# Optimization experiments

Hardware: AMD Instinct MI355X
Metric: run time of the kernel (lower is better)

Reference implementation:

```python
import jax, jax.numpy as jnp
import numpy as np

TAIL_BOUND = 3.0
MIN_BIN_W = 1e-3
MIN_BIN_H = 1e-3
MIN_DERIV = 1e-3


def _rq_spline_fwd(x, uw, uh, us):
    # unconstrained rational-quadratic spline (Durkan et al., 'linear' tails)
    # x: [N, C]; uw, uh: [C, B]; us: [C, B-1]
    C, B = uw.shape
    dt = x.dtype
    inside = (x >= -TAIL_BOUND) & (x <= TAIL_BOUND)
    xc = jnp.clip(x, -TAIL_BOUND, TAIL_BOUND)

    widths = MIN_BIN_W + (1.0 - MIN_BIN_W * B) * jax.nn.softmax(uw, axis=-1)
    cumw = jnp.concatenate([jnp.zeros((C, 1), dt), jnp.cumsum(widths, -1)], -1)
    cumw = 2.0 * TAIL_BOUND * cumw - TAIL_BOUND
    cumw = cumw.at[:, 0].set(-TAIL_BOUND).at[:, -1].set(TAIL_BOUND)
    widths = cumw[:, 1:] - cumw[:, :-1]

    heights = MIN_BIN_H + (1.0 - MIN_BIN_H * B) * jax.nn.softmax(uh, axis=-1)
    cumh = jnp.concatenate([jnp.zeros((C, 1), dt), jnp.cumsum(heights, -1)], -1)
    cumh = 2.0 * TAIL_BOUND * cumh - TAIL_BOUND
    cumh = cumh.at[:, 0].set(-TAIL_BOUND).at[:, -1].set(TAIL_BOUND)
    heights = cumh[:, 1:] - cumh[:, :-1]

    # boundary derivative logits -> softplus(const) = 1 - MIN_DERIV
    const = float(np.log(np.expm1(1.0 - MIN_DERIV)))
    ud = jnp.concatenate([jnp.full((C, 1), const, dt), us,
                          jnp.full((C, 1), const, dt)], -1)
    derivs = MIN_DERIV + jax.nn.softplus(ud)  # [C, B+1]

    # searchsorted on bin x-edges (eps shift on last edge, as in reference impl)
    edges = cumw.at[:, -1].add(1e-6)
    idx = jnp.clip(jnp.sum(xc[:, :, None] >= edges[None, :, :], -1) - 1, 0, B - 1)  # [N, C]

    ci = jnp.arange(C)[None, :]
    xk = cumw[ci, idx]
    wk = widths[ci, idx]
    yk = cumh[ci, idx]
    hk = heights[ci, idx]
    dk = derivs[ci, idx]
    dk1 = derivs[ci, idx + 1]
    delta = hk / wk

    theta = (xc - xk) / wk
    t1m = theta * (1.0 - theta)
    num = hk * (delta * theta * theta + dk * t1m)
    den = delta + (dk + dk1 - 2.0 * delta) * t1m
    y = yk + num / den
    dnum = delta * delta * (dk1 * theta * theta + 2.0 * delta * t1m
                            + dk * (1.0 - theta) * (1.0 - theta))
    logdet = jnp.log(dnum) - 2.0 * jnp.log(den)

    # identity (log-det 0) outside the interval
    return jnp.where(inside, y, x), jnp.where(inside, logdet, jnp.zeros_like(logdet))


def setup_inputs() -> dict:
    key = jax.random.key(0)
    ks = jax.random.split(key, 6)
    N, L, C, B = 1000000, 8, 8, 32
    return {
        "x": jax.random.normal(ks[0], (N,), jnp.float32),
        "w": jax.random.normal(ks[1], (L, C, B), jnp.float32),
        "h": jax.random.normal(ks[2], (L, C, B), jnp.float32),
        "s": jax.random.normal(ks[3], (L, C, B - 1), jnp.float32),
        "bias": jax.random.normal(ks[4], (L + 1, C), jnp.float32),
        "log_scale": jax.random.normal(ks[5], (L + 1, C), jnp.float32),
    }


def reference(x, w, h, s, bias, log_scale):
    L, C = w.shape[0], w.shape[1]
    z = jnp.broadcast_to(x[:, None], (x.shape[0], C))
    log_j = jnp.zeros_like(z)
    for step in range(L):
        z = (z - bias[step]) * jnp.exp(-log_scale[step])
        z, ld = _rq_spline_fwd(z, w[step], h[step], s[step])
        log_j = log_j + ld - log_scale[step]
    z = (z - bias[L]) * jnp.exp(-log_scale[L])
    return z, log_j - log_scale[L]
```

## Files before the change

### kernel.cpp

```cpp
#include <hip/hip_runtime.h>
#include <hip/hip_bf16.h>


#define TB 3.0f
#define NB 32
#define NC 8
#define NL 8
#define LN2 0.69314718055994530942f

#define GX0 -6.5f
#define GX1 6.5f
#define TZ 0.5f
#define TL 0.5f

#define PT_FLOATS (64 * 99)
#define GP_FLOATS (PT_FLOATS + 72 + 72 + 8)
#define GP_BYTES  (GP_FLOATS * 4)
#define TAB_OFF   26112

__device__ __forceinline__ float softplusf(float v) {
    return fmaxf(v, 0.f) + log1pf(expf(-fabsf(v)));
}

__device__ __forceinline__ unsigned short f2h(float f) {
    _Float16 h = (_Float16)f;
    unsigned short u;
    __builtin_memcpy(&u, &h, 2);
    return u;
}
__device__ __forceinline__ float h2f(unsigned short u) {
    _Float16 h;
    __builtin_memcpy(&h, &u, 2);
    return (float)h;
}

__device__ __forceinline__ int bsearch32(const float* __restrict__ E, float xc) {
    int i = (xc >= E[16]) ? 16 : 0;
    i += (xc >= E[i + 8]) ? 8 : 0;
    i += (xc >= E[i + 4]) ? 4 : 0;
    i += (xc >= E[i + 2]) ? 2 : 0;
    i += (xc >= E[i + 1]) ? 1 : 0;
    return i;
}

__device__ __forceinline__ void spline_eval(const float* __restrict__ Tlc,
                                            float zc, float& zo, float& ldo) {
    const float* E  = Tlc;
    const float* Hc = Tlc + 33;
    const float* Dv = Tlc + 66;

    float xc = fminf(fmaxf(zc, -TB), TB);
    int i = bsearch32(E, xc);

    float xk  = E[i],  xk1 = E[i + 1];
    float yk  = Hc[i], yk1 = Hc[i + 1];
    float dk  = Dv[i], dk1 = Dv[i + 1];

    float wk    = xk1 - xk;
    float hk    = yk1 - yk;
    float invw  = __builtin_amdgcn_rcpf(wk);
    float delta = hk * invw;
    float th    = (xc - xk) * invw;
    float omt   = 1.f - th;
    float t1m   = th * omt;
    float th2   = th * th;

    float num    = hk * fmaf(delta, th2, dk * t1m);
    float den    = fmaf(fmaf(-2.f, delta, dk + dk1), t1m, delta);
    float invden = __builtin_amdgcn_rcpf(den);
    float y      = fmaf(num, invden, yk);

    float dt    = delta * t1m;
    float inner = fmaf(dk1, th2, fmaf(dk, omt * omt, dt + dt));
    float dnum  = (delta * delta) * inner;
    float r  = dnum * invden * invden;
    float ld = LN2 * __builtin_amdgcn_logf(r);

    bool inside = (zc >= -TB) && (zc <= TB);
    zo  = inside ? y : zc;
    ldo = inside ? ld : 0.f;
}

extern "C" __global__ void __launch_bounds__(256)
build_tables(const float* __restrict__ w, const float* __restrict__ h,
             const float* __restrict__ s, const float* __restrict__ bias,
             const float* __restrict__ lsc, float* __restrict__ gparam)
{
    __shared__ float T[PT_FLOATS];
    __shared__ float Sc[72], Bb[72], LJ[8];

    const int tid = threadIdx.x;

    if (tid < 64) {
        const int l = tid >> 3, c = tid & 7;
        float* cw = &T[tid * 99];
        const float* wr = w + (l * NC + c) * NB;
        float m = wr[0];
        for (int b = 1; b < NB; ++b) m = fmaxf(m, wr[b]);
        float sum = 0.f;
        for (int b = 0; b < NB; ++b) sum += expf(wr[b] - m);
        float inv = 1.f / sum;
        float acc = 0.f;
        cw[0] = -TB;
        for (int b = 0; b < NB; ++b) {
            acc += 1e-3f + (1.f - 1e-3f * NB) * (expf(wr[b] - m) * inv);
            cw[b + 1] = 6.f * acc - 3.f;
        }
        cw[NB] = TB;
    } else if (tid < 128) {
        const int t = tid - 64;
        float* ch = &T[t * 99 + 33];
        const int l = t >> 3, c = t & 7;
        const float* hr = h + (l * NC + c) * NB;
        float m = hr[0];
        for (int b = 1; b < NB; ++b) m = fmaxf(m, hr[b]);
        float sum = 0.f;
        for (int b = 0; b < NB; ++b) sum += expf(hr[b] - m);
        float inv = 1.f / sum;
        float acc = 0.f;
        ch[0] = -TB;
        for (int b = 0; b < NB; ++b) {
            acc += 1e-3f + (1.f - 1e-3f * NB) * (expf(hr[b] - m) * inv);
            ch[b + 1] = 6.f * acc - 3.f;
        }
        ch[NB] = TB;
    } else if (tid < 192) {
        const int t = tid - 128;
        const int l = t >> 3, c = t & 7;
        float* dv = &T[t * 99 + 66];
        const float* sr = s + (l * NC + c) * (NB - 1);
        const float cst = logf(expm1f(1.f - 1e-3f));
        const float dbound = 1e-3f + softplusf(cst);
        dv[0]  = dbound;
        dv[NB] = dbound;
        for (int k = 0; k < NB - 1; ++k)
            dv[k + 1] = 1e-3f + softplusf(sr[k]);
    }
    if (tid < 72) { Sc[tid] = expf(-lsc[tid]); Bb[tid] = bias[tid]; }
    if (tid < 8) {
        float a = 0.f;
        for (int l = 0; l <= NL; ++l) a += lsc[l * NC + tid];
        LJ[tid] = -a;
    }
    __syncthreads();

    for (int k = tid; k < PT_FLOATS; k += 256) gparam[k] = T[k];
    if (tid < 72) gparam[PT_FLOATS + tid]       = Sc[tid];
    if (tid < 72) gparam[PT_FLOATS + 72 + tid]  = Bb[tid];
    if (tid < 8)  gparam[PT_FLOATS + 144 + tid] = LJ[tid];
}

extern "C" __global__ void __launch_bounds__(256)
grid_eval(const float* __restrict__ gparam, char* __restrict__ tabb,
          int G, float dx)
{
    __shared__ float T[GP_FLOATS];
    __shared__ unsigned short ZL[256 * 16];
    for (int k = threadIdx.x; k < GP_FLOATS; k += 256) T[k] = gparam[k];
    __syncthreads();
    const float* ScT = T + PT_FLOATS;
    const float* BbT = ScT + 72;
    const float* LJT = BbT + 72;

    const int t  = threadIdx.x;
    const int p0 = blockIdx.x * 255;
    const int i  = min(p0 + t, G - 1);

    const float xv = fmaf((float)i, dx, GX0);
    float z[NC], lj[NC];
#pragma unroll
    for (int c = 0; c < NC; ++c) { z[c] = xv; lj[c] = LJT[c]; }

#pragma unroll 1
    for (int l = 0; l < NL; ++l) {
        const float* Tl = T + l * NC * 99;
#pragma unroll
        for (int c = 0; c < NC; ++c) {
            float u = (z[c] - BbT[l * 8 + c]) * ScT[l * 8 + c];
            float zo, ld;
            spline_eval(Tl + c * 99, u, zo, ld);
            z[c] = zo;
            lj[c] += ld;
        }
    }
    unsigned short zh[NC], lh[NC];
#pragma unroll
    for (int c = 0; c < NC; ++c) {
        z[c] = (z[c] - BbT[NL * 8 + c]) * ScT[NL * 8 + c];
        zh[c] = f2h(z[c]);
        lh[c] = f2h(lj[c]);
        ZL[t * 16 + c]     = zh[c];
        ZL[t * 16 + 8 + c] = lh[c];
    }
    __syncthreads();

    const int r = p0 + t;
    if (t < 255 && r <= G - 2) {
        ushort4* rowp = (ushort4*)(tabb + (size_t)r * 64);
#pragma unroll
        for (int c = 0; c < NC; ++c) {
            const float zn  = h2f(ZL[(t + 1) * 16 + c]);
            const float ljn = h2f(ZL[(t + 1) * 16 + 8 + c]);
            ushort4 v;
            v.x = zh[c]; v.y = f2h(zn - h2f(zh[c]));
            v.z = lh[c]; v.w = f2h(ljn - h2f(lh[c]));
            rowp[c] = v;
        }
    }
}

extern "C" __global__ void __launch_bounds__(256)
interp_kernel(const float* __restrict__ x, const char* __restrict__ tabb,
              float* __restrict__ out,
              unsigned* __restrict__ wcnt, unsigned* __restrict__ wl,
              int N, int G, float dx, float invdx)
{
    const int n   = blockIdx.x * 256 + threadIdx.x;
    const int wid = n >> 6;
    if (n >= N) return;

    const float xv = x[n];
    int i = (int)floorf((xv - GX0) * invdx);
    const bool oor = !(xv > GX0 && xv < GX1);
    i = min(max(i, 0), G - 2);
    const float t = (xv - fmaf((float)i, dx, GX0)) * invdx;

    const float4* rp = (const float4*)(tabb + (size_t)i * 64);
    union { float4 q[4]; unsigned int u[16]; } R;
    R.q[0] = rp[0]; R.q[1] = rp[1]; R.q[2] = rp[2]; R.q[3] = rp[3];

    float z[NC], lj[NC];
    int flags = 0;
#pragma unroll
    for (int c = 0; c < NC; ++c) {
        const unsigned a = R.u[2 * c], b = R.u[2 * c + 1];
        const float z0 = h2f((unsigned short)a);
        const float dz = h2f((unsigned short)(a >> 16));
        const float l0 = h2f((unsigned short)b);
        const float dl = h2f((unsigned short)(b >> 16));
        z[c]  = fmaf(t, dz, z0);
        lj[c] = fmaf(t, dl, l0);
        if (fabsf(dz) > TZ || fabsf(dl) > TL) flags |= (1 << c);
    }
    if (oor) flags = 0xff;

    const unsigned long long act = __ballot(1);
    const unsigned long long m   = __ballot(flags != 0);
    const int lane = threadIdx.x & 63;
    if (flags) {
        const int rank = __popcll(m & ((1ull << lane) - 1ull));
        wl[(size_t)wid * 64 + rank] = ((unsigned)n << 8) | (unsigned)flags;
    }
    if (lane == __ffsll((long long)act) - 1)
        wcnt[wid] = (unsigned)__popcll(m);

    float4* oz = (float4*)(out + (size_t)n * NC);
    oz[0] = make_float4(z[0], z[1], z[2], z[3]);
    oz[1] = make_float4(z[4], z[5], z[6], z[7]);
    float4* ol = (float4*)(out + (size_t)N * NC + (size_t)n * NC);
    ol[0] = make_float4(lj[0], lj[1], lj[2], lj[3]);
    ol[1] = make_float4(lj[4], lj[5], lj[6], lj[7]);
}

extern "C" __global__ void __launch_bounds__(256)
exact_kernel(const float* __restrict__ x, const float* __restrict__ gparam,
             const unsigned* __restrict__ wcnt, const unsigned* __restrict__ wl,
             int nwl, float* __restrict__ out, int N)
{
    __shared__ float T[GP_FLOATS];
    for (int k = threadIdx.x; k < GP_FLOATS; k += 256) T[k] = gparam[k];
    __syncthreads();
    const float* ScT = T + PT_FLOATS;
    const float* BbT = ScT + 72;
    const float* LJT = BbT + 72;

    const int lane = threadIdx.x & 63;
    const int wloc = threadIdx.x >> 6;
    for (int W = blockIdx.x * 4 + wloc; W < nwl; W += (int)gridDim.x * 4) {
        const unsigned cnt = min(wcnt[W], 64u);
        for (unsigned p = 0; p < cnt; p += 8) {
            const unsigned eidx = p + (unsigned)(lane >> 3);
            if (eidx >= cnt) continue;
            const unsigned ent = wl[(size_t)W * 64 + eidx];
            const int c = lane & 7;
            if (!((ent >> c) & 1u)) continue;
            const int n = (int)(ent >> 8);
            if (n >= N) continue;
            const float xv = x[n];
            float zc = xv;
            float lacc = LJT[c];
#pragma unroll 1
            for (int l = 0; l < NL; ++l) {
                zc = (zc - BbT[l * 8 + c]) * ScT[l * 8 + c];
                float ld;
                spline_eval(T + (l * 8 + c) * 99, zc, zc, ld);
                lacc += ld;
            }
            zc = (zc - BbT[NL * 8 + c]) * ScT[NL * 8 + c];
            out[(size_t)n * NC + c] = zc;
            out[(size_t)N * NC + (size_t)n * NC + c] = lacc;
        }
    }
}

extern "C" __global__ void __launch_bounds__(256)
flow_kernel(const float* __restrict__ x, const float* __restrict__ w,
            const float* __restrict__ h, const float* __restrict__ s,
            const float* __restrict__ bias, const float* __restrict__ lsc,
            float* __restrict__ out, int N)
{
    __shared__ float T[PT_FLOATS];
    __shared__ float Bb[NL + 1][NC];
    __shared__ float Sc[NL + 1][NC];
    __shared__ float LJC[NC];

    const int tid = threadIdx.x;
    if (tid < 64) {
        const int l = tid >> 3, c = tid & 7;
        float* cw = &T[tid * 99];
        {
            const float* wr = w + (l * NC + c) * NB;
            float m = wr[0];
            for (int b = 1; b < NB; ++b) m = fmaxf(m, wr[b]);
            float sum = 0.f;
            for (int b = 0; b < NB; ++b) sum += expf(wr[b] - m);
            float inv = 1.f / sum;
            float acc = 0.f;
            cw[0] = -TB;
            for (int b = 0; b < NB; ++b) {
                acc += 1e-3f + (1.f - 1e-3f * NB) * (expf(wr[b] - m) * inv);
                cw[b + 1] = 6.f * acc - 3.f;
            }
            cw[NB] = TB;
        }
        {
            float* ch = cw + 33;
            const float* hr = h + (l * NC + c) * NB;
            float m = hr[0];
            for (int b = 1; b < NB; ++b) m = fmaxf(m, hr[b]);
            float sum = 0.f;
            for (int b = 0; b < NB; ++b) sum += expf(hr[b] - m);
            float inv = 1.f / sum;
            float acc = 0.f;
            ch[0] = -TB;
            for (int b = 0; b < NB; ++b) {
                acc += 1e-3f + (1.f - 1e-3f * NB) * (expf(hr[b] - m) * inv);
                ch[b + 1] = 6.f * acc - 3.f;
            }
            ch[NB] = TB;
        }
        {
            float* dv = cw + 66;
            const float* sr = s + (l * NC + c) * (NB - 1);
            const float cst = logf(expm1f(1.f - 1e-3f));
            const float dbound = 1e-3f + softplusf(cst);
            dv[0]  = dbound;
            dv[NB] = dbound;
            for (int k = 0; k < NB - 1; ++k)
                dv[k + 1] = 1e-3f + softplusf(sr[k]);
        }
    }
    if (tid < (NL + 1) * NC) {
        const int l = tid >> 3, c = tid & 7;
        Bb[l][c] = bias[tid];
        Sc[l][c] = expf(-lsc[tid]);
    }
    if (tid < NC) {
        float a = 0.f;
        for (int l = 0; l <= NL; ++l) a += lsc[l * NC + tid];
        LJC[tid] = -a;
    }
    __syncthreads();

    const int n = blockIdx.x * 256 + tid;
    if (n >= N) return;
    const float xv = x[n];
    float z[NC], lj[NC];
#pragma unroll
    for (int c = 0; c < NC; ++c) { z[c] = xv; lj[c] = LJC[c]; }
#pragma unroll 1
    for (int l = 0; l < NL; ++l) {
        const float* Tl = &T[l * NC * 99];
#pragma unroll
        for (int c = 0; c < NC; ++c) {
            float zc = (z[c] - Bb[l][c]) * Sc[l][c];
            float zo, ld;
            spline_eval(Tl + c * 99, zc, zo, ld);
            z[c] = zo;
            lj[c] += ld;
        }
    }
#pragma unroll
    for (int c = 0; c < NC; ++c) z[c] = (z[c] - Bb[NL][c]) * Sc[NL][c];

    float4* oz = (float4*)(out + (size_t)n * NC);
    oz[0] = make_float4(z[0], z[1], z[2], z[3]);
    oz[1] = make_float4(z[4], z[5], z[6], z[7]);
    float4* ol = (float4*)(out + (size_t)N * NC + (size_t)n * NC);
    ol[0] = make_float4(lj[0], lj[1], lj[2], lj[3]);
    ol[1] = make_float4(lj[4], lj[5], lj[6], lj[7]);
}

extern "C" void kernel_launch(void* const* d_in, const int* in_sizes, int n_in,
                              void* d_out, int out_size, void* d_ws, size_t ws_size,
                              hipStream_t stream) {
    const float* x    = (const float*)d_in[0];
    const float* w    = (const float*)d_in[1];
    const float* h    = (const float*)d_in[2];
    const float* s    = (const float*)d_in[3];
    const float* bias = (const float*)d_in[4];
    const float* lsc  = (const float*)d_in[5];
    float* out = (float*)d_out;
    const int N = in_sizes[0];

    const int nwl = (N + 63) / 64;
    int G = 65536;
    while (G > 2048 &&
           ((size_t)TAB_OFF + (size_t)G * 64 + (size_t)nwl * 260) > ws_size)
        G >>= 1;
    const size_t tabEnd = (size_t)TAB_OFF + (size_t)G * 64;
    const size_t need   = tabEnd + (size_t)nwl * 260;

    if (need <= ws_size) {
        char* basep = (char*)d_ws;
        float*    gparam = (float*)basep;
        char*     tabb   = basep + TAB_OFF;
        unsigned* wcnt   = (unsigned*)(basep + tabEnd);
        unsigned* wl     = (unsigned*)(basep + tabEnd + (size_t)nwl * 4);

        const float dx = (GX1 - GX0) / (float)(G - 1);
        const int gblocks = (G - 1 + 254) / 255;
        build_tables<<<1, 256, 0, stream>>>(w, h, s, bias, lsc, gparam);
        grid_eval<<<gblocks, 256, 0, stream>>>(gparam, tabb, G, dx);
        interp_kernel<<<(N + 255) / 256, 256, 0, stream>>>(
            x, tabb, out, wcnt, wl, N, G, dx, 1.f / dx);
        exact_kernel<<<(nwl + 3) / 4, 256, 0, stream>>>(
            x, gparam, wcnt, wl, nwl, out, N);
    } else {
        flow_kernel<<<(N + 255) / 256, 256, 0, stream>>>(
            x, w, h, s, bias, lsc, out, N);
    }
}
```

Before: 70.90 us.

## Fuse exact fallback into interp kernel with block-local per-channel compaction

Measured after the change: 63.91 us. 9.9% less time.

```diff
diff --git a/kernel.cpp b/kernel.cpp
--- a/kernel.cpp
+++ b/kernel.cpp
@@ -17,6 +17,7 @@
 #define GP_FLOATS (PT_FLOATS + 72 + 72 + 8)
 #define GP_BYTES  (GP_FLOATS * 4)
 #define TAB_OFF   26112
+#define CAP 256
 
 __device__ __forceinline__ float softplusf(float v) {
     return fmaxf(v, 0.f) + log1pf(expf(-fabsf(v)));
@@ -79,6 +80,25 @@
     bool inside = (zc >= -TB) && (zc <= TB);
     zo  = inside ? y : zc;
     ldo = inside ? ld : 0.f;
+}
+
+__device__ __forceinline__ void exact_chain(const float* __restrict__ T,
+                                            float xv, int c,
+                                            float& zout, float& lout) {
+    const float* ScT = T + PT_FLOATS;
+    const float* BbT = ScT + 72;
+    const float* LJT = BbT + 72;
+    float zc = xv;
+    float lacc = LJT[c];
+#pragma unroll 1
+    for (int l = 0; l < NL; ++l) {
+        zc = (zc - BbT[l * 8 + c]) * ScT[l * 8 + c];
+        float ld;
+        spline_eval(T + (l * 8 + c) * 99, zc, zc, ld);
+        lacc += ld;
+    }
+    zout = (zc - BbT[NL * 8 + c]) * ScT[NL * 8 + c];
+    lout = lacc;
 }
 
 extern "C" __global__ void __launch_bounds__(256)
@@ -211,95 +231,117 @@
 
 extern "C" __global__ void __launch_bounds__(256)
 interp_kernel(const float* __restrict__ x, const char* __restrict__ tabb,
-              float* __restrict__ out,
-              unsigned* __restrict__ wcnt, unsigned* __restrict__ wl,
+              const float* __restrict__ gparam, float* __restrict__ out,
               int N, int G, float dx, float invdx)
 {
-    const int n   = blockIdx.x * 256 + threadIdx.x;
-    const int wid = n >> 6;
-    if (n >= N) return;
-
-    const float xv = x[n];
-    int i = (int)floorf((xv - GX0) * invdx);
-    const bool oor = !(xv > GX0 && xv < GX1);
-    i = min(max(i, 0), G - 2);
-    const float t = (xv - fmaf((float)i, dx, GX0)) * invdx;
-
-    const float4* rp = (const float4*)(tabb + (size_t)i * 64);
-    union { float4 q[4]; unsigned int u[16]; } R;
-    R.q[0] = rp[0]; R.q[1] = rp[1]; R.q[2] = rp[2]; R.q[3] = rp[3];
+    __shared__ float T[GP_FLOATS];
+    __shared__ float xbuf[256];
+    __shared__ unsigned short pairs[CAP];
+    __shared__ float resZ[CAP], resL[CAP];
+    __shared__ unsigned wsum[4];
+
+    const int tid  = threadIdx.x;
+    const int n    = blockIdx.x * 256 + tid;
+    const int lane = tid & 63;
+    const int wloc = tid >> 6;
+    const bool active = (n < N);
+
+    float xv = 0.f;
+    if (active) xv = x[n];
+    xbuf[tid] = xv;
 
     float z[NC], lj[NC];
     int flags = 0;
+    if (active) {
+        int i = (int)floorf((xv - GX0) * invdx);
+        const bool oor = !(xv > GX0 && xv < GX1);
+        i = min(max(i, 0), G - 2);
+        const float t = (xv - fmaf((float)i, dx, GX0)) * invdx;
+
+        const float4* rp = (const float4*)(tabb + (size_t)i * 64);
+        union { float4 q[4]; unsigned int u[16]; } R;
+        R.q[0] = rp[0]; R.q[1] = rp[1]; R.q[2] = rp[2]; R.q[3] = rp[3];
+#pragma unroll
+        for (int c = 0; c < NC; ++c) {
+            const unsigned a = R.u[2 * c], b = R.u[2 * c + 1];
+            const float z0 = h2f((unsigned short)a);
+            const float dz = h2f((unsigned short)(a >> 16));
+            const float l0 = h2f((unsigned short)b);
+            const float dl = h2f((unsigned short)(b >> 16));
+            z[c]  = fmaf(t, dz, z0);
+            lj[c] = fmaf(t, dl, l0);
+            if (fabsf(dz) > TZ || fabsf(dl) > TL) flags |= (1 << c);
+        }
+        if (oor) flags = 0xff;
+    }
+
+    unsigned long long m[NC];
+    unsigned wtot = 0;
 #pragma unroll
     for (int c = 0; c < NC; ++c) {
-        const unsigned a = R.u[2 * c], b = R.u[2 * c + 1];
-        const float z0 = h2f((unsigned short)a);
-        const float dz = h2f((unsigned short)(a >> 16));
-        const float l0 = h2f((unsigned short)b);
-        const float dl = h2f((unsigned short)(b >> 16));
-        z[c]  = fmaf(t, dz, z0);
-        lj[c] = fmaf(t, dl, l0);
-        if (fabsf(dz) > TZ || fabsf(dl) > TL) flags |= (1 << c);
-    }
-    if (oor) flags = 0xff;
-
-    const unsigned long long act = __ballot(1);
-    const unsigned long long m   = __ballot(flags != 0);
-    const int lane = threadIdx.x & 63;
-    if (flags) {
-        const int rank = __popcll(m & ((1ull << lane) - 1ull));
-        wl[(size_t)wid * 64 + rank] = ((unsigned)n << 8) | (unsigned)flags;
-    }
-    if (lane == __ffsll((long long)act) - 1)
-        wcnt[wid] = (unsigned)__popcll(m);
-
-    float4* oz = (float4*)(out + (size_t)n * NC);
-    oz[0] = make_float4(z[0], z[1], z[2], z[3]);
-    oz[1] = make_float4(z[4], z[5], z[6], z[7]);
-    float4* ol = (float4*)(out + (size_t)N * NC + (size_t)n * NC);
-    ol[0] = make_float4(lj[0], lj[1], lj[2], lj[3]);
-    ol[1] = make_float4(lj[4], lj[5], lj[6], lj[7]);
-}
-
-extern "C" __global__ void __launch_bounds__(256)
-exact_kernel(const float* __restrict__ x, const float* __restrict__ gparam,
-             const unsigned* __restrict__ wcnt, const unsigned* __restrict__ wl,
-             int nwl, float* __restrict__ out, int N)
-{
-    __shared__ float T[GP_FLOATS];
-    for (int k = threadIdx.x; k < GP_FLOATS; k += 256) T[k] = gparam[k];
-    __syncthreads();
-    const float* ScT = T + PT_FLOATS;
-    const float* BbT = ScT + 72;
-    const float* LJT = BbT + 72;
-
-    const int lane = threadIdx.x & 63;
-    const int wloc = threadIdx.x >> 6;
-    for (int W = blockIdx.x * 4 + wloc; W < nwl; W += (int)gridDim.x * 4) {
-        const unsigned cnt = min(wcnt[W], 64u);
-        for (unsigned p = 0; p < cnt; p += 8) {
-            const unsigned eidx = p + (unsigned)(lane >> 3);
-            if (eidx >= cnt) continue;
-            const unsigned ent = wl[(size_t)W * 64 + eidx];
-            const int c = lane & 7;
-            if (!((ent >> c) & 1u)) continue;
-            const int n = (int)(ent >> 8);
-            if (n >= N) continue;
-            const float xv = x[n];
-            float zc = xv;
-            float lacc = LJT[c];
-#pragma unroll 1
-            for (int l = 0; l < NL; ++l) {
-                zc = (zc - BbT[l * 8 + c]) * ScT[l * 8 + c];
-                float ld;
-                spline_eval(T + (l * 8 + c) * 99, zc, zc, ld);
-                lacc += ld;
+        m[c] = __ballot((flags >> c) & 1);
+        wtot += (unsigned)__popcll(m[c]);
+    }
+    if (lane == 0) wsum[wloc] = wtot;
+    __syncthreads();
+
+    unsigned woff = 0, btot = 0;
+#pragma unroll
+    for (int j = 0; j < 4; ++j) {
+        const unsigned v = wsum[j];
+        if (j < wloc) woff += v;
+        btot += v;
+    }
+    const unsigned long long lowmask = (1ull << lane) - 1ull;
+    {
+        unsigned basec = 0;
+#pragma unroll
+        for (int c = 0; c < NC; ++c) {
+            if ((flags >> c) & 1) {
+                const unsigned idx = woff + basec + (unsigned)__popcll(m[c] & lowmask);
+                if (idx < CAP) pairs[idx] = (unsigned short)((tid << 3) | c);
             }
-            zc = (zc - BbT[NL * 8 + c]) * ScT[NL * 8 + c];
-            out[(size_t)n * NC + c] = zc;
-            out[(size_t)N * NC + (size_t)n * NC + c] = lacc;
-        }
+            basec += (unsigned)__popcll(m[c]);
+        }
+    }
+    if (btot > 0) {
+        for (int k = tid; k < GP_FLOATS; k += 256) T[k] = gparam[k];
+    }
+    __syncthreads();
+
+    const unsigned pcnt = min(btot, (unsigned)CAP);
+    for (unsigned k = tid; k < pcnt; k += 256) {
+        const unsigned pr = pairs[k];
+        const int stid = (int)(pr >> 3), c = (int)(pr & 7u);
+        float zo, lo;
+        exact_chain(T, xbuf[stid], c, zo, lo);
+        resZ[k] = zo; resL[k] = lo;
+    }
+    __syncthreads();
+
+    if (active && flags) {
+        unsigned basec = 0;
+#pragma unroll
+        for (int c = 0; c < NC; ++c) {
+            if ((flags >> c) & 1) {
+                const unsigned idx = woff + basec + (unsigned)__popcll(m[c] & lowmask);
+                if (idx < CAP) {
+                    z[c] = resZ[idx]; lj[c] = resL[idx];
+                } else {
+                    exact_chain(T, xv, c, z[c], lj[c]);
+                }
+            }
+            basec += (unsigned)__popcll(m[c]);
+        }
+    }
+
+    if (active) {
+        float4* oz = (float4*)(out + (size_t)n * NC);
+        oz[0] = make_float4(z[0], z[1], z[2], z[3]);
+        oz[1] = make_float4(z[4], z[5], z[6], z[7]);
+        float4* ol = (float4*)(out + (size_t)N * NC + (size_t)n * NC);
+        ol[0] = make_float4(lj[0], lj[1], lj[2], lj[3]);
+        ol[1] = make_float4(lj[4], lj[5], lj[6], lj[7]);
     }
 }
 
@@ -413,29 +455,22 @@
     float* out = (float*)d_out;
     const int N = in_sizes[0];
 
-    const int nwl = (N + 63) / 64;
     int G = 65536;
-    while (G > 2048 &&
-           ((size_t)TAB_OFF + (size_t)G * 64 + (size_t)nwl * 260) > ws_size)
+    while (G > 2048 && ((size_t)TAB_OFF + (size_t)G * 64) > ws_size)
         G >>= 1;
-    const size_t tabEnd = (size_t)TAB_OFF + (size_t)G * 64;
-    const size_t need   = tabEnd + (size_t)nwl * 260;
+    const size_t need = (size_t)TAB_OFF + (size_t)G * 64;
 
     if (need <= ws_size) {
         char* basep = (char*)d_ws;
-        float*    gparam = (float*)basep;
-        char*     tabb   = basep + TAB_OFF;
-        unsigned* wcnt   = (unsigned*)(basep + tabEnd);
-        unsigned* wl     = (unsigned*)(basep + tabEnd + (size_t)nwl * 4);
+        float* gparam = (float*)basep;
+        char*  tabb   = basep + TAB_OFF;
 
         const float dx = (GX1 - GX0) / (float)(G - 1);
         const int gblocks = (G - 1 + 254) / 255;
         build_tables<<<1, 256, 0, stream>>>(w, h, s, bias, lsc, gparam);
         grid_eval<<<gblocks, 256, 0, stream>>>(gparam, tabb, G, dx);
         interp_kernel<<<(N + 255) / 256, 256, 0, stream>>>(
-            x, tabb, out, wcnt, wl, N, G, dx, 1.f / dx);
-        exact_kernel<<<(nwl + 3) / 4, 256, 0, stream>>>(
-            x, gparam, wcnt, wl, nwl, out, N);
+            x, tabb, gparam, out, N, G, dx, 1.f / dx);
     } else {
         flow_kernel<<<(N + 255) / 256, 256, 0, stream>>>(
             x, w, h, s, bias, lsc, out, N);
```

## Split interpolation and exact fallback work per point-channel pair

Applied to the files above, without the earlier changes.

Measured after the change: 98.83 us. 39.4% more time.

```diff
diff --git a/kernel.cpp b/kernel.cpp
--- a/kernel.cpp
+++ b/kernel.cpp
@@ -79,6 +79,25 @@
     bool inside = (zc >= -TB) && (zc <= TB);
     zo  = inside ? y : zc;
     ldo = inside ? ld : 0.f;
+}
+
+__device__ __forceinline__ void exact_chain(const float* __restrict__ T,
+                                            float xv, int c,
+                                            float& zout, float& lout) {
+    const float* ScT = T + PT_FLOATS;
+    const float* BbT = ScT + 72;
+    const float* LJT = BbT + 72;
+    float zc = xv;
+    float lacc = LJT[c];
+#pragma unroll 1
+    for (int l = 0; l < NL; ++l) {
+        zc = (zc - BbT[l * 8 + c]) * ScT[l * 8 + c];
+        float ld;
+        spline_eval(T + (l * 8 + c) * 99, zc, zc, ld);
+        lacc += ld;
+    }
+    zout = (zc - BbT[NL * 8 + c]) * ScT[NL * 8 + c];
+    lout = lacc;
 }
 
 extern "C" __global__ void __launch_bounds__(256)
@@ -215,51 +234,45 @@
               unsigned* __restrict__ wcnt, unsigned* __restrict__ wl,
               int N, int G, float dx, float invdx)
 {
-    const int n   = blockIdx.x * 256 + threadIdx.x;
-    const int wid = n >> 6;
-    if (n >= N) return;
-
-    const float xv = x[n];
-    int i = (int)floorf((xv - GX0) * invdx);
-    const bool oor = !(xv > GX0 && xv < GX1);
-    i = min(max(i, 0), G - 2);
-    const float t = (xv - fmaf((float)i, dx, GX0)) * invdx;
-
-    const float4* rp = (const float4*)(tabb + (size_t)i * 64);
-    union { float4 q[4]; unsigned int u[16]; } R;
-    R.q[0] = rp[0]; R.q[1] = rp[1]; R.q[2] = rp[2]; R.q[3] = rp[3];
-
-    float z[NC], lj[NC];
-    int flags = 0;
-#pragma unroll
-    for (int c = 0; c < NC; ++c) {
-        const unsigned a = R.u[2 * c], b = R.u[2 * c + 1];
-        const float z0 = h2f((unsigned short)a);
-        const float dz = h2f((unsigned short)(a >> 16));
-        const float l0 = h2f((unsigned short)b);
-        const float dl = h2f((unsigned short)(b >> 16));
-        z[c]  = fmaf(t, dz, z0);
-        lj[c] = fmaf(t, dl, l0);
-        if (fabsf(dz) > TZ || fabsf(dl) > TL) flags |= (1 << c);
-    }
-    if (oor) flags = 0xff;
-
-    const unsigned long long act = __ballot(1);
-    const unsigned long long m   = __ballot(flags != 0);
+    const int gt   = blockIdx.x * 256 + threadIdx.x;
+    const int p    = gt >> 3;
+    const int c    = gt & 7;
     const int lane = threadIdx.x & 63;
-    if (flags) {
+    const int wid  = gt >> 6;
+    const bool active = (p < N);
+
+    float zv = 0.f, lv = 0.f;
+    bool flag = false;
+    float xv = 0.f;
+    if (active) {
+        xv = x[p];
+        int i = (int)floorf((xv - GX0) * invdx);
+        const bool oor = !(xv > GX0 && xv < GX1);
+        i = min(max(i, 0), G - 2);
+        const float t = (xv - fmaf((float)i, dx, GX0)) * invdx;
+
+        const uint2 ab = *(const uint2*)(tabb + (size_t)i * 64 + c * 8);
+        const float z0 = h2f((unsigned short)ab.x);
+        const float dz = h2f((unsigned short)(ab.x >> 16));
+        const float l0 = h2f((unsigned short)ab.y);
+        const float dl = h2f((unsigned short)(ab.y >> 16));
+        zv = fmaf(t, dz, z0);
+        lv = fmaf(t, dl, l0);
+        flag = oor || (fabsf(dz) > TZ) || (fabsf(dl) > TL);
+    }
+
+    const unsigned long long m = __ballot(flag);
+    if (flag) {
         const int rank = __popcll(m & ((1ull << lane) - 1ull));
-        wl[(size_t)wid * 64 + rank] = ((unsigned)n << 8) | (unsigned)flags;
-    }
-    if (lane == __ffsll((long long)act) - 1)
+        wl[(size_t)wid * 64 + rank] = ((unsigned)p << 3) | (unsigned)c;
+    }
+    if (lane == 0)
         wcnt[wid] = (unsigned)__popcll(m);
 
-    float4* oz = (float4*)(out + (size_t)n * NC);
-    oz[0] = make_float4(z[0], z[1], z[2], z[3]);
-    oz[1] = make_float4(z[4], z[5], z[6], z[7]);
-    float4* ol = (float4*)(out + (size_t)N * NC + (size_t)n * NC);
-    ol[0] = make_float4(lj[0], lj[1], lj[2], lj[3]);
-    ol[1] = make_float4(lj[4], lj[5], lj[6], lj[7]);
+    if (active) {
+        out[(size_t)p * NC + c] = zv;
+        out[(size_t)N * NC + (size_t)p * NC + c] = lv;
+    }
 }
 
 extern "C" __global__ void __launch_bounds__(256)
@@ -270,35 +283,21 @@
     __shared__ float T[GP_FLOATS];
     for (int k = threadIdx.x; k < GP_FLOATS; k += 256) T[k] = gparam[k];
     __syncthreads();
-    const float* ScT = T + PT_FLOATS;
-    const float* BbT = ScT + 72;
-    const float* LJT = BbT + 72;
 
     const int lane = threadIdx.x & 63;
     const int wloc = threadIdx.x >> 6;
     for (int W = blockIdx.x * 4 + wloc; W < nwl; W += (int)gridDim.x * 4) {
         const unsigned cnt = min(wcnt[W], 64u);
-        for (unsigned p = 0; p < cnt; p += 8) {
-            const unsigned eidx = p + (unsigned)(lane >> 3);
-            if (eidx >= cnt) continue;
-            const unsigned ent = wl[(size_t)W * 64 + eidx];
-            const int c = lane & 7;
-            if (!((ent >> c) & 1u)) continue;
-            const int n = (int)(ent >> 8);
-            if (n >= N) continue;
-            const float xv = x[n];
-            float zc = xv;
-            float lacc = LJT[c];
-#pragma unroll 1
-            for (int l = 0; l < NL; ++l) {
-                zc = (zc - BbT[l * 8 + c]) * ScT[l * 8 + c];
-                float ld;
-                spline_eval(T + (l * 8 + c) * 99, zc, zc, ld);
-                lacc += ld;
+        if (lane < (int)cnt) {
+            const unsigned ent = wl[(size_t)W * 64 + lane];
+            const int n = (int)(ent >> 3);
+            const int c = (int)(ent & 7u);
+            if (n < N) {
+                float zo, lo;
+                exact_chain(T, x[n], c, zo, lo);
+                out[(size_t)n * NC + c] = zo;
+                out[(size_t)N * NC + (size_t)n * NC + c] = lo;
             }
-            zc = (zc - BbT[NL * 8 + c]) * ScT[NL * 8 + c];
-            out[(size_t)n * NC + c] = zc;
-            out[(size_t)N * NC + (size_t)n * NC + c] = lacc;
         }
     }
 }
@@ -413,7 +412,7 @@
     float* out = (float*)d_out;
     const int N = in_sizes[0];
 
-    const int nwl = (N + 63) / 64;
+    const int nwl = (N + 7) / 8;
     int G = 65536;
     while (G > 2048 &&
            ((size_t)TAB_OFF + (size_t)G * 64 + (size_t)nwl * 260) > ws_size)
@@ -430,11 +429,12 @@
 
         const float dx = (GX1 - GX0) / (float)(G - 1);
         const int gblocks = (G - 1 + 254) / 255;
+        const int iblocks = (int)(((long long)N * 8 + 255) / 256);
         build_tables<<<1, 256, 0, stream>>>(w, h, s, bias, lsc, gparam);
         grid_eval<<<gblocks, 256, 0, stream>>>(gparam, tabb, G, dx);
-        interp_kernel<<<(N + 255) / 256, 256, 0, stream>>>(
+        interp_kernel<<<iblocks, 256, 0, stream>>>(
             x, tabb, out, wcnt, wl, N, G, dx, 1.f / dx);
-        exact_kernel<<<(nwl + 3) / 4, 256, 0, stream>>>(
+        exact_kernel<<<512, 256, 0, stream>>>(
             x, gparam, wcnt, wl, nwl, out, N);
     } else {
         flow_kernel<<<(N + 255) / 256, 256, 0, stream>>>(
```
